# Optimization experiments

Measured on AMD Instinct MI355X. Metric: run time of the kernel, lower is better.

Reference implementation:

```python
import jax, jax.numpy as jnp
import numpy as np

EPS = 1e-12  # torch F.normalize clamps the norm at 1e-12

def _l2norm(v, axis):
    n = jnp.sqrt(jnp.sum(v * v, axis=axis, keepdims=True))
    return v / jnp.maximum(n, EPS)

def setup_inputs() -> dict:
    key = jax.random.key(0)
    k1, k2, k3, k4 = jax.random.split(key, 4)
    N, C, H, W, K = 64, 64, 64, 64, 128
    alpha = 1.0
    x = jax.random.normal(k1, (N, C, H, W), dtype=jnp.float32)
    centroids = jax.random.uniform(k2, (K, C), dtype=jnp.float32)
    # conv is initialized from centroids (2*alpha*c, -alpha*||c||) but is an
    # independent parameter after init; keep the init relationship for realism.
    conv_w = 2.0 * alpha * centroids
    conv_b = -alpha * jnp.sqrt(jnp.sum(centroids * centroids, axis=1))
    return {"x": x, "centroids": centroids, "conv_w": conv_w, "conv_b": conv_b}

def reference(x, centroids, conv_w, conv_b):
    N, C, H, W = x.shape
    K = centroids.shape[0]
    # L2-normalize descriptors along channel dim
    xn = _l2norm(x, axis=1)                                   # [N,C,H,W]
    # 1x1 conv == per-pixel linear map C->K
    logits = jnp.einsum('nchw,kc->nkhw', xn, conv_w) + conv_b[None, :, None, None]
    sa = jax.nn.softmax(logits.reshape(N, K, H * W), axis=1)  # [N,K,HW]
    xf = xn.reshape(N, C, H * W)                              # [N,C,HW]
    # vlad[n,k,c] = sum_l sa[n,k,l] * (xf[n,c,l] - centroids[k,c])
    #            = (sa @ xf^T)[n,k,c] - sum_l sa[n,k,l] * centroids[k,c]
    vlad = jnp.einsum('nkl,ncl->nkc', sa, xf) - sa.sum(axis=-1)[:, :, None] * centroids[None]
    vlad = _l2norm(vlad, axis=2)            # intra-normalization per cluster
    vlad = vlad.reshape(N, K * C)
    vlad = _l2norm(vlad, axis=1)            # global L2 normalization
    return vlad
```

## Files before the change

kernel.cpp:

```cpp
#include <hip/hip_runtime.h>
#include <math.h>

#define NIMG   64
#define CDIM   64
#define HWPX   4096
#define PARTS  8
#define KCL    128
#define PIXPART (HWPX / PARTS)
#define TL     32
#define NCHUNK (PIXPART / TL)
#define SHIFT  10.0f
#define RSQRT128 0.08838834764831845f

#define XP_S 72
#define XC_S 40
#define PH_S 40

typedef __attribute__((ext_vector_type(8))) short short8;
typedef __attribute__((ext_vector_type(4))) float f32x4;

#define MFMA(a, b, c) __builtin_amdgcn_mfma_f32_16x16x32_bf16((a), (b), (c), 0, 0, 0)

__device__ __forceinline__ void tsplit(float f, short& hs, short& ls) {
    unsigned u = __builtin_bit_cast(unsigned, f);
    hs = (short)(u >> 16);
    float hf = __builtin_bit_cast(float, u & 0xffff0000u);
    ls = (short)(__builtin_bit_cast(unsigned, f - hf) >> 16);
}

__global__ __launch_bounds__(256, 2)
void netvlad_main(const float* __restrict__ x,
                  const float* __restrict__ conv_w,
                  const float* __restrict__ conv_b,
                  float* __restrict__ vout,
                  float* __restrict__ asout,
                  int use_atomic)
{
    __shared__ __align__(16) short xp_hi[TL * XP_S],  xp_lo[TL * XP_S];
    __shared__ __align__(16) short xc_hi[CDIM * XC_S], xc_lo[CDIM * XC_S];
    __shared__ __align__(16) short ph_hi[KCL * PH_S],  ph_lo[KCL * PH_S];
    __shared__ float redA[4 * 33];
    __shared__ float sumP[4 * TL];

    const int t   = threadIdx.x;
    const int w   = t >> 6;
    const int l   = t & 63;
    const int l15 = l & 15, l4 = l >> 4;
    const int n    = blockIdx.x >> 3;
    const int part = blockIdx.x & 7;
    const int p_s  = t & 31;
    const int sg   = t >> 5;

    short8 wh[2][2], wl[2][2];
    #pragma unroll
    for (int kt = 0; kt < 2; ++kt) {
        const int krow = (2 * w + kt) * 16 + l15;
        #pragma unroll
        for (int ks = 0; ks < 2; ++ks) {
            const float4* wp = (const float4*)(conv_w + krow * CDIM + ks * 32 + l4 * 8);
            float4 wa = wp[0], wb = wp[1];
            float wv[8] = {wa.x, wa.y, wa.z, wa.w, wb.x, wb.y, wb.z, wb.w};
            #pragma unroll
            for (int j = 0; j < 8; ++j) {
                short hs, ls; tsplit(wv[j], hs, ls);
                wh[kt][ks][j] = hs; wl[kt][ks][j] = ls;
            }
        }
    }
    float cbr[2][4];
    #pragma unroll
    for (int kt = 0; kt < 2; ++kt)
        #pragma unroll
        for (int i = 0; i < 4; ++i)
            cbr[kt][i] = conv_b[(2 * w + kt) * 16 + l4 * 4 + i] - SHIFT;

    f32x4 acc2[2][4];
    #pragma unroll
    for (int a = 0; a < 2; ++a)
        #pragma unroll
        for (int b = 0; b < 4; ++b) acc2[a][b] = (f32x4)0.0f;
    float asr[2][4];
    #pragma unroll
    for (int a = 0; a < 2; ++a)
        #pragma unroll
        for (int i = 0; i < 4; ++i) asr[a][i] = 0.f;

    const float* xbase = x + (size_t)n * CDIM * HWPX + part * PIXPART;

    float xv[8];
    #pragma unroll
    for (int j = 0; j < 8; ++j)
        xv[j] = xbase[(sg * 8 + j) * HWPX + p_s];

    for (int ch = 0; ch < NCHUNK; ++ch) {
        float ssq = 0.f;
        #pragma unroll
        for (int j = 0; j < 8; ++j) ssq += xv[j] * xv[j];
        ssq += __shfl_xor(ssq, 32);
        if (l < 32) redA[w * 33 + p_s] = ssq;

        short8 vh, vl;
        #pragma unroll
        for (int j = 0; j < 8; ++j) {
            short hs, ls; tsplit(xv[j], hs, ls);
            vh[j] = hs; vl[j] = ls;
            xc_hi[(sg * 8 + j) * XC_S + p_s] = hs;
            xc_lo[(sg * 8 + j) * XC_S + p_s] = ls;
        }
        *(short8*)&xp_hi[p_s * XP_S + sg * 8] = vh;
        *(short8*)&xp_lo[p_s * XP_S + sg * 8] = vl;
        __syncthreads();

        if (ch + 1 < NCHUNK) {
            #pragma unroll
            for (int j = 0; j < 8; ++j)
                xv[j] = xbase[(sg * 8 + j) * HWPX + (ch + 1) * TL + p_s];
        }

        f32x4 a1[2][2];
        #pragma unroll
        for (int a = 0; a < 2; ++a)
            #pragma unroll
            for (int b = 0; b < 2; ++b) a1[a][b] = (f32x4)0.0f;
        #pragma unroll
        for (int ks = 0; ks < 2; ++ks) {
            #pragma unroll
            for (int pt = 0; pt < 2; ++pt) {
                short8 bh = *(short8*)&xp_hi[(pt * 16 + l15) * XP_S + ks * 32 + l4 * 8];
                short8 bl = *(short8*)&xp_lo[(pt * 16 + l15) * XP_S + ks * 32 + l4 * 8];
                #pragma unroll
                for (int kt = 0; kt < 2; ++kt) {
                    a1[kt][pt] = MFMA(wh[kt][ks], bh, a1[kt][pt]);
                    a1[kt][pt] = MFMA(wh[kt][ks], bl, a1[kt][pt]);
                    a1[kt][pt] = MFMA(wl[kt][ks], bh, a1[kt][pt]);
                }
            }
        }

        float rn[2];
        #pragma unroll
        for (int pt = 0; pt < 2; ++pt) {
            const int col = pt * 16 + l15;
            float s0 = redA[col] + redA[33 + col];
            float s1 = redA[2 * 33 + col] + redA[3 * 33 + col];
            rn[pt] = 1.0f / fmaxf(sqrtf(s0 + s1), 1e-12f);
        }

        float e[2][2][4], sp[2] = {0.f, 0.f};
        #pragma unroll
        for (int kt = 0; kt < 2; ++kt)
            #pragma unroll
            for (int pt = 0; pt < 2; ++pt)
                #pragma unroll
                for (int i = 0; i < 4; ++i) {
                    float ev = __expf(fmaf(a1[kt][pt][i], rn[pt], cbr[kt][i]));
                    e[kt][pt][i] = ev;
                    sp[pt] += ev;
                }
        #pragma unroll
        for (int pt = 0; pt < 2; ++pt) {
            sp[pt] += __shfl_xor(sp[pt], 16);
            sp[pt] += __shfl_xor(sp[pt], 32);
        }
        if (l4 == 0) {
            sumP[w * TL + l15]      = sp[0];
            sumP[w * TL + 16 + l15] = sp[1];
        }
        __syncthreads();

        float rden[2], rdn2[2];
        #pragma unroll
        for (int pt = 0; pt < 2; ++pt) {
            const int col = pt * 16 + l15;
            float den = sumP[col] + sumP[TL + col] + sumP[2 * TL + col] + sumP[3 * TL + col];
            rden[pt] = 1.0f / den;
            rdn2[pt] = rden[pt] * rn[pt];
        }

        #pragma unroll
        for (int kt = 0; kt < 2; ++kt)
            #pragma unroll
            for (int i = 0; i < 4; ++i) {
                const int row = (2 * w + kt) * 16 + l4 * 4 + i;
                #pragma unroll
                for (int pt = 0; pt < 2; ++pt) {
                    float ev = e[kt][pt][i];
                    asr[kt][i] = fmaf(ev, rden[pt], asr[kt][i]);
                    float Pn = ev * rdn2[pt];
                    short hs, ls; tsplit(Pn, hs, ls);
                    ph_hi[row * PH_S + pt * 16 + l15] = hs;
                    ph_lo[row * PH_S + pt * 16 + l15] = ls;
                }
            }

        {
            short8 xh2[4], xl2[4];
            #pragma unroll
            for (int ct = 0; ct < 4; ++ct) {
                xh2[ct] = *(short8*)&xc_hi[(ct * 16 + l15) * XC_S + l4 * 8];
                xl2[ct] = *(short8*)&xc_lo[(ct * 16 + l15) * XC_S + l4 * 8];
            }
            #pragma unroll
            for (int kt = 0; kt < 2; ++kt) {
                short8 ah = *(short8*)&ph_hi[((2 * w + kt) * 16 + l15) * PH_S + l4 * 8];
                short8 al = *(short8*)&ph_lo[((2 * w + kt) * 16 + l15) * PH_S + l4 * 8];
                #pragma unroll
                for (int ct = 0; ct < 4; ++ct) {
                    acc2[kt][ct] = MFMA(ah, xh2[ct], acc2[kt][ct]);
                    acc2[kt][ct] = MFMA(ah, xl2[ct], acc2[kt][ct]);
                    acc2[kt][ct] = MFMA(al, xh2[ct], acc2[kt][ct]);
                }
            }
        }
        __syncthreads();
    }

    float* vg = use_atomic ? vout + (size_t)n * KCL * CDIM
                           : vout + (size_t)(n * PARTS + part) * KCL * CDIM;
    #pragma unroll
    for (int kt = 0; kt < 2; ++kt)
        #pragma unroll
        for (int ct = 0; ct < 4; ++ct)
            #pragma unroll
            for (int i = 0; i < 4; ++i) {
                const int row = (2 * w + kt) * 16 + l4 * 4 + i;
                const int col = ct * 16 + l15;
                if (use_atomic) atomicAdd(&vg[row * CDIM + col], acc2[kt][ct][i]);
                else            vg[row * CDIM + col] = acc2[kt][ct][i];
            }

    #pragma unroll
    for (int kt = 0; kt < 2; ++kt)
        #pragma unroll
        for (int i = 0; i < 4; ++i) {
            float v = asr[kt][i];
            v += __shfl_xor(v, 1); v += __shfl_xor(v, 2);
            v += __shfl_xor(v, 4); v += __shfl_xor(v, 8);
            if (l15 == 0) {
                const int row = (2 * w + kt) * 16 + l4 * 4 + i;
                if (use_atomic) atomicAdd(&asout[n * KCL + row], v);
                else            asout[(n * PARTS + part) * KCL + row] = v;
            }
        }
}

__global__ __launch_bounds__(256)
void netvlad_finalize(const float* __restrict__ vpart,
                      const float* __restrict__ aspart,
                      const float* __restrict__ cent,
                      float* __restrict__ out,
                      int nparts)
{
    const int t = threadIdx.x;
    const int n  = blockIdx.x >> 3;
    const int kg = blockIdx.x & 7;
    const int k  = kg * 16 + (t >> 4);
    const int c0 = (t & 15) * 4;

    float vsum[4] = {0.f, 0.f, 0.f, 0.f};
    float av = 0.f;
    for (int pt = 0; pt < nparts; ++pt) {
        const float* vg = vpart + (((size_t)n * nparts + pt) * KCL + k) * CDIM + c0;
        float4 a = *(const float4*)vg;
        vsum[0] += a.x; vsum[1] += a.y; vsum[2] += a.z; vsum[3] += a.w;
        av += aspart[(n * nparts + pt) * KCL + k];
    }

    float4 cq = *(const float4*)(cent + k * CDIM + c0);
    float cc[4] = {cq.x, cq.y, cq.z, cq.w};
    float ss = 0.f;
    #pragma unroll
    for (int j = 0; j < 4; ++j) {
        vsum[j] -= av * cc[j];
        ss += vsum[j] * vsum[j];
    }
    ss += __shfl_xor(ss, 1); ss += __shfl_xor(ss, 2);
    ss += __shfl_xor(ss, 4); ss += __shfl_xor(ss, 8);
    const float s = (1.0f / fmaxf(sqrtf(ss), 1e-12f)) * RSQRT128;

    float4 o;
    o.x = vsum[0] * s; o.y = vsum[1] * s; o.z = vsum[2] * s; o.w = vsum[3] * s;
    *(float4*)(out + (size_t)n * KCL * CDIM + k * CDIM + c0) = o;
}

extern "C" void kernel_launch(void* const* d_in, const int* in_sizes, int n_in,
                              void* d_out, int out_size, void* d_ws, size_t ws_size,
                              hipStream_t stream) {
    const float* x     = (const float*)d_in[0];
    const float* cent  = (const float*)d_in[1];
    const float* convw = (const float*)d_in[2];
    const float* convb = (const float*)d_in[3];
    float* out = (float*)d_out;

    const size_t needP = (size_t)NIMG * PARTS * (KCL * CDIM + KCL) * sizeof(float);
    int nparts, use_atomic;
    if (ws_size >= needP) { nparts = PARTS; use_atomic = 0; }
    else                  { nparts = 1;     use_atomic = 1; }

    float* vws  = (float*)d_ws;
    float* asws = vws + (size_t)NIMG * nparts * KCL * CDIM;
    if (use_atomic) {
        const size_t zb = (size_t)NIMG * (KCL * CDIM + KCL) * sizeof(float);
        hipMemsetAsync(d_ws, 0, zb, stream);
    }

    netvlad_main<<<dim3(NIMG * PARTS), dim3(256), 0, stream>>>(x, convw, convb, vws, asws, use_atomic);
    netvlad_finalize<<<dim3(NIMG * 8), dim3(256), 0, stream>>>(vws, asws, cent, out, nparts);
}
```

Baseline: 134.6 us.

## Double-buffer staged chunk tiles and cut per-chunk barriers to one

```diff
diff --git a/kernel.cpp b/kernel.cpp
--- a/kernel.cpp
+++ b/kernel.cpp
@@ -36,11 +36,11 @@
                   float* __restrict__ asout,
                   int use_atomic)
 {
-    __shared__ __align__(16) short xp_hi[TL * XP_S],  xp_lo[TL * XP_S];
-    __shared__ __align__(16) short xc_hi[CDIM * XC_S], xc_lo[CDIM * XC_S];
+    __shared__ __align__(16) short xp_hi[2][TL * XP_S],  xp_lo[2][TL * XP_S];
+    __shared__ __align__(16) short xc_hi[2][CDIM * XC_S], xc_lo[2][CDIM * XC_S];
     __shared__ __align__(16) short ph_hi[KCL * PH_S],  ph_lo[KCL * PH_S];
-    __shared__ float redA[4 * 33];
-    __shared__ float sumP[4 * TL];
+    __shared__ float redA[2][4 * 33];
+    __shared__ float sumP[2][4 * TL];
 
     const int t   = threadIdx.x;
     const int w   = t >> 6;
@@ -87,30 +87,33 @@
 
     const float* xbase = x + (size_t)n * CDIM * HWPX + part * PIXPART;
 
-    float xv[8];
-    #pragma unroll
-    for (int j = 0; j < 8; ++j)
-        xv[j] = xbase[(sg * 8 + j) * HWPX + p_s];
+    {
+        float xv0[8], ssq = 0.f;
+        #pragma unroll
+        for (int j = 0; j < 8; ++j) {
+            xv0[j] = xbase[(sg * 8 + j) * HWPX + p_s];
+            ssq += xv0[j] * xv0[j];
+        }
+        ssq += __shfl_xor(ssq, 32);
+        if (l < 32) redA[0][w * 33 + p_s] = ssq;
+        short8 vh, vl;
+        #pragma unroll
+        for (int j = 0; j < 8; ++j) {
+            short hs, ls; tsplit(xv0[j], hs, ls);
+            vh[j] = hs; vl[j] = ls;
+            xc_hi[0][(sg * 8 + j) * XC_S + p_s] = hs;
+            xc_lo[0][(sg * 8 + j) * XC_S + p_s] = ls;
+        }
+        *(short8*)&xp_hi[0][p_s * XP_S + sg * 8] = vh;
+        *(short8*)&xp_lo[0][p_s * XP_S + sg * 8] = vl;
+    }
+    __syncthreads();
 
     for (int ch = 0; ch < NCHUNK; ++ch) {
-        float ssq = 0.f;
-        #pragma unroll
-        for (int j = 0; j < 8; ++j) ssq += xv[j] * xv[j];
-        ssq += __shfl_xor(ssq, 32);
-        if (l < 32) redA[w * 33 + p_s] = ssq;
-
-        short8 vh, vl;
-        #pragma unroll
-        for (int j = 0; j < 8; ++j) {
-            short hs, ls; tsplit(xv[j], hs, ls);
-            vh[j] = hs; vl[j] = ls;
-            xc_hi[(sg * 8 + j) * XC_S + p_s] = hs;
-            xc_lo[(sg * 8 + j) * XC_S + p_s] = ls;
-        }
-        *(short8*)&xp_hi[p_s * XP_S + sg * 8] = vh;
-        *(short8*)&xp_lo[p_s * XP_S + sg * 8] = vl;
-        __syncthreads();
-
+        const int b  = ch & 1;
+        const int bn = b ^ 1;
+
+        float xv[8];
         if (ch + 1 < NCHUNK) {
             #pragma unroll
             for (int j = 0; j < 8; ++j)
@@ -121,13 +124,13 @@
         #pragma unroll
         for (int a = 0; a < 2; ++a)
             #pragma unroll
-            for (int b = 0; b < 2; ++b) a1[a][b] = (f32x4)0.0f;
+            for (int b2 = 0; b2 < 2; ++b2) a1[a][b2] = (f32x4)0.0f;
         #pragma unroll
         for (int ks = 0; ks < 2; ++ks) {
             #pragma unroll
             for (int pt = 0; pt < 2; ++pt) {
-                short8 bh = *(short8*)&xp_hi[(pt * 16 + l15) * XP_S + ks * 32 + l4 * 8];
-                short8 bl = *(short8*)&xp_lo[(pt * 16 + l15) * XP_S + ks * 32 + l4 * 8];
+                short8 bh = *(short8*)&xp_hi[b][(pt * 16 + l15) * XP_S + ks * 32 + l4 * 8];
+                short8 bl = *(short8*)&xp_lo[b][(pt * 16 + l15) * XP_S + ks * 32 + l4 * 8];
                 #pragma unroll
                 for (int kt = 0; kt < 2; ++kt) {
                     a1[kt][pt] = MFMA(wh[kt][ks], bh, a1[kt][pt]);
@@ -141,8 +144,8 @@
         #pragma unroll
         for (int pt = 0; pt < 2; ++pt) {
             const int col = pt * 16 + l15;
-            float s0 = redA[col] + redA[33 + col];
-            float s1 = redA[2 * 33 + col] + redA[3 * 33 + col];
+            float s0 = redA[b][col] + redA[b][33 + col];
+            float s1 = redA[b][2 * 33 + col] + redA[b][3 * 33 + col];
             rn[pt] = 1.0f / fmaxf(sqrtf(s0 + s1), 1e-12f);
         }
 
@@ -163,20 +166,46 @@
             sp[pt] += __shfl_xor(sp[pt], 32);
         }
         if (l4 == 0) {
-            sumP[w * TL + l15]      = sp[0];
-            sumP[w * TL + 16 + l15] = sp[1];
-        }
+            sumP[b][w * TL + l15]      = sp[0];
+            sumP[b][w * TL + 16 + l15] = sp[1];
+        }
+
+        if (ch + 1 < NCHUNK) {
+            float ssq = 0.f;
+            #pragma unroll
+            for (int j = 0; j < 8; ++j) ssq += xv[j] * xv[j];
+            ssq += __shfl_xor(ssq, 32);
+            if (l < 32) redA[bn][w * 33 + p_s] = ssq;
+            short8 vh, vl;
+            #pragma unroll
+            for (int j = 0; j < 8; ++j) {
+                short hs, ls; tsplit(xv[j], hs, ls);
+                vh[j] = hs; vl[j] = ls;
+                xc_hi[bn][(sg * 8 + j) * XC_S + p_s] = hs;
+                xc_lo[bn][(sg * 8 + j) * XC_S + p_s] = ls;
+            }
+            *(short8*)&xp_hi[bn][p_s * XP_S + sg * 8] = vh;
+            *(short8*)&xp_lo[bn][p_s * XP_S + sg * 8] = vl;
+        }
+
+        short8 xh2[4], xl2[4];
+        #pragma unroll
+        for (int ct = 0; ct < 4; ++ct) {
+            xh2[ct] = *(short8*)&xc_hi[b][(ct * 16 + l15) * XC_S + l4 * 8];
+            xl2[ct] = *(short8*)&xc_lo[b][(ct * 16 + l15) * XC_S + l4 * 8];
+        }
+
         __syncthreads();
 
         float rden[2], rdn2[2];
         #pragma unroll
         for (int pt = 0; pt < 2; ++pt) {
             const int col = pt * 16 + l15;
-            float den = sumP[col] + sumP[TL + col] + sumP[2 * TL + col] + sumP[3 * TL + col];
+            float den = sumP[b][col] + sumP[b][TL + col]
+                      + sumP[b][2 * TL + col] + sumP[b][3 * TL + col];
             rden[pt] = 1.0f / den;
             rdn2[pt] = rden[pt] * rn[pt];
         }
-
         #pragma unroll
         for (int kt = 0; kt < 2; ++kt)
             #pragma unroll
@@ -193,26 +222,17 @@
                 }
             }
 
-        {
-            short8 xh2[4], xl2[4];
+        #pragma unroll
+        for (int kt = 0; kt < 2; ++kt) {
+            short8 ah = *(short8*)&ph_hi[((2 * w + kt) * 16 + l15) * PH_S + l4 * 8];
+            short8 al = *(short8*)&ph_lo[((2 * w + kt) * 16 + l15) * PH_S + l4 * 8];
             #pragma unroll
             for (int ct = 0; ct < 4; ++ct) {
-                xh2[ct] = *(short8*)&xc_hi[(ct * 16 + l15) * XC_S + l4 * 8];
-                xl2[ct] = *(short8*)&xc_lo[(ct * 16 + l15) * XC_S + l4 * 8];
-            }
-            #pragma unroll
-            for (int kt = 0; kt < 2; ++kt) {
-                short8 ah = *(short8*)&ph_hi[((2 * w + kt) * 16 + l15) * PH_S + l4 * 8];
-                short8 al = *(short8*)&ph_lo[((2 * w + kt) * 16 + l15) * PH_S + l4 * 8];
-                #pragma unroll
-                for (int ct = 0; ct < 4; ++ct) {
-                    acc2[kt][ct] = MFMA(ah, xh2[ct], acc2[kt][ct]);
-                    acc2[kt][ct] = MFMA(ah, xl2[ct], acc2[kt][ct]);
-                    acc2[kt][ct] = MFMA(al, xh2[ct], acc2[kt][ct]);
-                }
-            }
-        }
-        __syncthreads();
+                acc2[kt][ct] = MFMA(ah, xh2[ct], acc2[kt][ct]);
+                acc2[kt][ct] = MFMA(ah, xl2[ct], acc2[kt][ct]);
+                acc2[kt][ct] = MFMA(al, xh2[ct], acc2[kt][ct]);
+            }
+        }
     }
 
     float* vg = use_atomic ? vout + (size_t)n * KCL * CDIM
```

New measurement: 135.3 us. Within noise of the previous version (+0.5%).
